# Optimization experiments

Measured on AMD Instinct MI355X. Metric: run time of the kernel, lower is better.

Reference implementation:

```python
import jax, jax.numpy as jnp
import numpy as np

B, S, H = 2, 2048, 2048
NH, NKV, HD = 16, 4, 128
ROPE_BASE = 10000.0


def hbit_linear(x, w):
    # BitNet: 8-bit per-token absmax activation quant, ternary (2-bit) weight quant
    s = 127.0 / jnp.clip(jnp.max(jnp.abs(x), axis=-1, keepdims=True), 1e-5, None)
    xq = jnp.clip(jnp.round(x * s), -128, 127) / s
    ws = 1.0 / jnp.clip(jnp.mean(jnp.abs(w)), 1e-5, None)
    wq = jnp.clip(jnp.round(w * ws), -1, 1) / ws
    return xq @ wq.T


def rotate_half(x):
    h = x.shape[-1] // 2
    return jnp.concatenate([-x[..., h:], x[..., :h]], axis=-1)


def rope_cos_sin(position_ids, head_dim, dtype):
    inv_freq = 1.0 / (ROPE_BASE ** (jnp.arange(0, head_dim, 2, dtype=jnp.float32) / head_dim))
    freqs = position_ids.astype(jnp.float32)[..., None] * inv_freq[None, None, :]  # (b,s,hd/2)
    emb = jnp.concatenate([freqs, freqs], axis=-1)  # (b,s,hd)
    return jnp.cos(emb).astype(dtype)[:, :, None, :], jnp.sin(emb).astype(dtype)[:, :, None, :]


def setup_inputs() -> dict:
    key = jax.random.key(0)
    ks = jax.random.split(key, 5)
    xavier = lambda k, shp: jax.random.uniform(k, shp, jnp.float32, -1.0, 1.0) * np.sqrt(6.0 / (shp[0] + shp[1]))
    causal = jnp.where(jnp.tril(jnp.ones((S, S), bool)), 0.0, -1e9).astype(jnp.float32)[None, None]
    return {
        "hidden_states": jax.random.normal(ks[0], (B, S, H), jnp.float32),
        "attention_mask": causal,
        "Wq": xavier(ks[1], (H, H)),
        "Wk": xavier(ks[2], (NKV * HD, H)),
        "Wv": xavier(ks[3], (NKV * HD, H)),
        "Wo": xavier(ks[4], (H, H)),
        "position_ids": jnp.arange(S, dtype=jnp.int64 if jax.config.jax_enable_x64 else jnp.int32)[None, :],
    }


def reference(hidden_states, attention_mask, Wq, Wk, Wv, Wo, position_ids):
    b, s, _ = hidden_states.shape
    q = hbit_linear(hidden_states, Wq).reshape(b, s, NH, HD)
    k = hbit_linear(hidden_states, Wk).reshape(b, s, NKV, HD)
    v = hbit_linear(hidden_states, Wv).reshape(b, s, NKV, HD)
    cos, sin = rope_cos_sin(position_ids, HD, q.dtype)  # (1,s,1,hd)
    q = q * cos + rotate_half(q) * sin
    k = k * cos + rotate_half(k) * sin
    n_rep = NH // NKV
    k = jnp.repeat(k, n_rep, axis=2)  # (b,s,NH,hd)
    v = jnp.repeat(v, n_rep, axis=2)
    scale = 1.0 / np.sqrt(HD)
    scores = jnp.einsum("bqhd,bkhd->bhqk", q, k) * scale + attention_mask
    probs = jax.nn.softmax(scores, axis=-1)  # dropout inactive (eval)
    out = jnp.einsum("bhqk,bkhd->bqhd", probs, v).reshape(b, s, NH * HD)
    return hbit_linear(out, Wo)
```

## Files before the change

### kernel.cpp

```cpp
#include <hip/hip_runtime.h>
#include <hip/hip_bf16.h>

#define B_ 2
#define S_ 2048
#define H_ 2048
#define NH_ 16
#define NKV_ 4
#define HD_ 128
#define M_ (B_*S_)
#define KVD_ (NKV_*HD_)

typedef signed char s8;
typedef __attribute__((ext_vector_type(8))) short short8;
typedef __attribute__((ext_vector_type(4))) float f32x4;
typedef __attribute__((ext_vector_type(4))) int int4v;

__device__ __forceinline__ float loadf(const void* p, long i, int isb){
  if (isb) return __bfloat162float(((const __hip_bfloat16*)p)[i]);
  return ((const float*)p)[i];
}

__device__ __forceinline__ unsigned short f2bf(float f){
  union { float f; unsigned u; } v; v.f = f;
  unsigned r = v.u + 0x7FFF + ((v.u >> 16) & 1);
  return (unsigned short)(r >> 16);
}

__device__ __forceinline__ float bf2f(unsigned short b){
  union { unsigned u; float f; } v; v.u = ((unsigned)b) << 16; return v.f;
}

__device__ __forceinline__ void gl2lds16(const void* g, void* l){
  __builtin_amdgcn_global_load_lds(
      (const __attribute__((address_space(1))) void*)g,
      (__attribute__((address_space(3))) void*)l, 16, 0, 0);
}

__global__ void k_detect(const unsigned int* x, int* flag){
  __shared__ int sh[256];
  int t = threadIdx.x, c = 0;
  for (int i = t; i < 2048; i += 256){
    unsigned e = (x[i] >> 7) & 0xFF;
    if (e >= 90 && e <= 150) c++;
  }
  sh[t] = c; __syncthreads();
  for (int k = 128; k > 0; k >>= 1){ if (t < k) sh[t] += sh[t+k]; __syncthreads(); }
  if (t == 0) flag[0] = (sh[0] > 1228) ? 1 : 0;
}

__global__ void k_prep(const void* Wq, const void* Wk, const void* Wv, const void* Wo,
                       const int* flag, float* wsum, float* ct, float* st){
  int bid = blockIdx.x, t = threadIdx.x;
  if (t < 64){
    float inv = exp2f(-(float)t * 0.20762050593045952f);
    float a = (float)bid * inv;
    float sn, cs; sincosf(a, &sn, &cs);
    ct[bid*64 + t] = cs; st[bid*64 + t] = sn;
  }
  __shared__ float sh[256];
  int isb = *flag;
  const void* w; long n; int wi; long b0; int nb;
  if (bid < 768)       { w = Wq; wi = 0; n = (long)H_*H_;   b0 = bid;      nb = 768; }
  else if (bid < 1024) { w = Wk; wi = 1; n = (long)KVD_*H_; b0 = bid-768;  nb = 256; }
  else if (bid < 1280) { w = Wv; wi = 2; n = (long)KVD_*H_; b0 = bid-1024; nb = 256; }
  else                 { w = Wo; wi = 3; n = (long)H_*H_;   b0 = bid-1280; nb = 768; }
  float s = 0.f;
  for (long i = b0*256 + t; i < n; i += (long)nb*256) s += fabsf(loadf(w, i, isb));
  sh[t] = s; __syncthreads();
  for (int k = 128; k > 0; k >>= 1){ if (t < k) sh[t] += sh[t+k]; __syncthreads(); }
  if (t == 0) atomicAdd(&wsum[wi], sh[0]);
}

__global__ void k_wquant_all(const void* Wq, const void* Wk, const void* Wv, const void* Wo,
                             const int* flag, const float* wsum,
                             s8* oq, s8* ok, s8* ov, s8* oo){
  int isb = *flag;
  int bid = blockIdx.x, t = threadIdx.x;
  const float cntq = (float)((long)H_*H_), cntkv = (float)((long)KVD_*H_);
  const void* w; s8* out; long n; int wi; long b0; int nb; float cnt;
  if (bid < 1024)      { w = Wq; out = oq; wi = 0; n = (long)H_*H_;   b0 = bid;       nb = 1024; cnt = cntq; }
  else if (bid < 1280) { w = Wk; out = ok; wi = 1; n = (long)KVD_*H_; b0 = bid-1024;  nb = 256;  cnt = cntkv; }
  else if (bid < 1536) { w = Wv; out = ov; wi = 2; n = (long)KVD_*H_; b0 = bid-1280;  nb = 256;  cnt = cntkv; }
  else                 { w = Wo; out = oo; wi = 3; n = (long)H_*H_;   b0 = bid-1536;  nb = 1024; cnt = cntq; }
  float mean = fmaxf(wsum[wi] / cnt, 1e-5f);
  float sc = 1.0f / mean;
  for (long i = b0*256 + t; i < n; i += (long)nb*256){
    float v = rintf(loadf(w, i, isb) * sc);
    v = fminf(fmaxf(v, -1.f), 1.f);
    out[i] = (s8)v;
  }
}

__global__ void k_aquant_in(const void* x, const int* flag, float* srow, s8* xq){
  __shared__ float sh[256];
  int isb = *flag; int r = blockIdx.x, t = threadIdx.x;
  long base = (long)r * H_;
  float v[8];
  if (isb){
    uint4 wv = ((const uint4*)((const unsigned short*)x + base))[t];
    unsigned u[4] = {wv.x, wv.y, wv.z, wv.w};
    #pragma unroll
    for (int i = 0; i < 4; i++){
      v[2*i]   = bf2f((unsigned short)(u[i] & 0xFFFF));
      v[2*i+1] = bf2f((unsigned short)(u[i] >> 16));
    }
  } else {
    const float4* p = (const float4*)((const float*)x + base);
    float4 a = p[t*2], b2 = p[t*2+1];
    v[0]=a.x; v[1]=a.y; v[2]=a.z; v[3]=a.w; v[4]=b2.x; v[5]=b2.y; v[6]=b2.z; v[7]=b2.w;
  }
  float mx = 0.f;
  #pragma unroll
  for (int i = 0; i < 8; i++) mx = fmaxf(mx, fabsf(v[i]));
  sh[t] = mx; __syncthreads();
  for (int k = 128; k > 0; k >>= 1){ if (t < k) sh[t] = fmaxf(sh[t], sh[t+k]); __syncthreads(); }
  float s = 127.0f / fmaxf(sh[0], 1e-5f);
  if (t == 0) srow[r] = s;
  unsigned long long pk = 0;
  #pragma unroll
  for (int i = 0; i < 8; i++){
    float q = fminf(fmaxf(rintf(v[i] * s), -128.f), 127.f);
    pk |= ((unsigned long long)(unsigned char)(s8)q) << (8*i);
  }
  *(unsigned long long*)(xq + base + t*8) = pk;
}

__global__ void k_aquant_bf16(const unsigned short* __restrict__ x, float* __restrict__ srow, s8* __restrict__ xq){
  __shared__ float sh[256];
  int r = blockIdx.x, t = threadIdx.x;
  long base = (long)r * H_;
  uint4 wv = ((const uint4*)(x + base))[t];
  unsigned u[4] = {wv.x, wv.y, wv.z, wv.w};
  float v[8];
  #pragma unroll
  for (int i = 0; i < 4; i++){
    v[2*i]   = bf2f((unsigned short)(u[i] & 0xFFFF));
    v[2*i+1] = bf2f((unsigned short)(u[i] >> 16));
  }
  float mx = 0.f;
  #pragma unroll
  for (int i = 0; i < 8; i++) mx = fmaxf(mx, fabsf(v[i]));
  sh[t] = mx; __syncthreads();
  for (int k = 128; k > 0; k >>= 1){ if (t < k) sh[t] = fmaxf(sh[t], sh[t+k]); __syncthreads(); }
  float s = 127.0f / fmaxf(sh[0], 1e-5f);
  if (t == 0) srow[r] = s;
  unsigned long long pk = 0;
  #pragma unroll
  for (int i = 0; i < 8; i++){
    float q = fminf(fmaxf(rintf(v[i] * s), -128.f), 127.f);
    pk |= ((unsigned long long)(unsigned char)(s8)q) << (8*i);
  }
  *(unsigned long long*)(xq + base + t*8) = pk;
}

__device__ __forceinline__ void gemm_core(
      const s8* __restrict__ A, const s8* __restrict__ Bw, s8* As, s8* Bs,
      const float* __restrict__ srow, float mean,
      void* __restrict__ Cout, int N, int mode, int isb,
      unsigned short* __restrict__ Vt,
      const float* __restrict__ ct, const float* __restrict__ st,
      long bcol, long arow){
  int tid = threadIdx.x;
  int wave = tid >> 6, lane = tid & 63;
  int quad = lane >> 4, c = lane & 15;
  int wm = wave >> 1, wn = wave & 1;
  const int K = H_;

  int4v acc[4][4];
  #pragma unroll
  for (int mt = 0; mt < 4; mt++)
    #pragma unroll
    for (int nt = 0; nt < 4; nt++) acc[mt][nt] = (int4v){0,0,0,0};

  int rl = lane >> 2;
  int kq = (lane & 3) ^ ((lane >> 3) & 3);
  int ch0 = wave*2, ch1 = wave*2 + 1;
  long gA0 = (arow + ch0*16 + rl)*(long)K + kq*16;
  long gA1 = (arow + ch1*16 + rl)*(long)K + kq*16;
  long gB0 = (bcol + ch0*16 + rl)*(long)K + kq*16;
  long gB1 = (bcol + ch1*16 + rl)*(long)K + kq*16;

  int sA = quad ^ ((c >> 1) & 3);
  int ntl[4];
  #pragma unroll
  for (int nt = 0; nt < 4; nt++) ntl[nt] = 2*wn + (nt & 1) + 4*(nt >> 1);
  int frA[4], frB[4];
  #pragma unroll
  for (int mt = 0; mt < 4; mt++) frA[mt] = (wm*64 + mt*16 + c)*64 + sA*16;
  #pragma unroll
  for (int nt = 0; nt < 4; nt++) frB[nt] = (ntl[nt]*16 + c)*64 + sA*16;

  for (int k0 = 0; k0 < K; k0 += 64){
    gl2lds16(A  + gA0 + k0, As + ch0*1024);
    gl2lds16(A  + gA1 + k0, As + ch1*1024);
    gl2lds16(Bw + gB0 + k0, Bs + ch0*1024);
    gl2lds16(Bw + gB1 + k0, Bs + ch1*1024);
    __syncthreads();
    int4v afr[4], bfr[4];
    #pragma unroll
    for (int mt = 0; mt < 4; mt++) afr[mt] = *(const int4v*)&As[frA[mt]];
    #pragma unroll
    for (int nt = 0; nt < 4; nt++) bfr[nt] = *(const int4v*)&Bs[frB[nt]];
    #pragma unroll
    for (int mt = 0; mt < 4; mt++)
      #pragma unroll
      for (int nt = 0; nt < 4; nt++)
        acc[mt][nt] = __builtin_amdgcn_mfma_i32_16x16x64_i8(afr[mt], bfr[nt], acc[mt][nt], 0, 0, 0);
    __syncthreads();
  }

  if (mode == 0 || mode == 3){
    unsigned short* Ob = (unsigned short*)Cout;
    #pragma unroll
    for (int mt = 0; mt < 4; mt++){
      #pragma unroll
      for (int r = 0; r < 4; r++){
        long grow = arow + wm*64 + mt*16 + quad*4 + r;
        float sc = mean / srow[grow];
        if (mode == 0) sc *= 0.12751743f;
        int pos = (int)(grow & (S_-1));
        #pragma unroll
        for (int p = 0; p < 2; p++){
          int col_lo = (int)bcol + (2*wn + p)*16 + c;
          int d = col_lo & 63;
          float cv = ct[pos*64 + d], sv = st[pos*64 + d];
          float vlo = acc[mt][p][r]   * sc;
          float vhi = acc[mt][p+2][r] * sc;
          Ob[grow*(long)N + col_lo]      = f2bf(vlo*cv - vhi*sv);
          Ob[grow*(long)N + col_lo + 64] = f2bf(vhi*cv + vlo*sv);
        }
      }
    }
  } else if (mode == 1){
    #pragma unroll
    for (int mt = 0; mt < 4; mt++){
      #pragma unroll
      for (int r = 0; r < 4; r++){
        long grow = arow + wm*64 + mt*16 + quad*4 + r;
        float sc = mean / srow[grow];
        long bb = grow >> 11; int sI = (int)(grow & (S_-1));
        unsigned short* base = Vt + bb*(long)KVD_*S_ + sI;
        #pragma unroll
        for (int nt = 0; nt < 4; nt++)
          base[(long)(bcol + ntl[nt]*16 + c)*S_] = f2bf(acc[mt][nt][r] * sc);
      }
    }
  } else {
    #pragma unroll
    for (int mt = 0; mt < 4; mt++){
      #pragma unroll
      for (int r = 0; r < 4; r++){
        long grow = arow + wm*64 + mt*16 + quad*4 + r;
        float sc = mean / srow[grow];
        long cb = grow*(long)N + bcol + c;
        if (isb){
          __hip_bfloat16* o = (__hip_bfloat16*)Cout;
          #pragma unroll
          for (int nt = 0; nt < 4; nt++)
            o[cb + ntl[nt]*16] = __float2bfloat16(acc[mt][nt][r] * sc);
        } else {
          float* o = (float*)Cout;
          #pragma unroll
          for (int nt = 0; nt < 4; nt++)
            o[cb + ntl[nt]*16] = acc[mt][nt][r] * sc;
        }
      }
    }
  }
}

__global__ __launch_bounds__(256, 2) void k_gemm_qkv(
      const s8* __restrict__ xq,
      const s8* __restrict__ wqq, const s8* __restrict__ wkq, const s8* __restrict__ wvq,
      const float* __restrict__ srow, const float* __restrict__ wsum,
      unsigned short* __restrict__ Qb, unsigned short* __restrict__ Kb,
      unsigned short* __restrict__ Vt,
      const float* __restrict__ ct, const float* __restrict__ st){
  __shared__ __align__(16) s8 As[128*64];
  __shared__ __align__(16) s8 Bs[128*64];
  int lid = blockIdx.x;
  int xcd = lid & 7;
  int rem = lid >> 3;
  int by  = xcd*4 + (rem & 3);
  int bx  = rem >> 2;
  const float cntq = (float)((long)H_*H_), cntkv = (float)((long)KVD_*H_);
  const s8* Bw; void* Cout; unsigned short* vt = nullptr;
  int N, mode; float mean; long bcol;
  if (bx < 16){
    Bw = wqq; Cout = Qb; N = H_;   mode = 0; mean = fmaxf(wsum[0]/cntq, 1e-5f);  bcol = (long)bx*128;
  } else if (bx < 20){
    Bw = wkq; Cout = Kb; N = KVD_; mode = 3; mean = fmaxf(wsum[1]/cntkv, 1e-5f); bcol = (long)(bx-16)*128;
  } else {
    Bw = wvq; Cout = nullptr; vt = Vt; N = KVD_; mode = 1; mean = fmaxf(wsum[2]/cntkv, 1e-5f); bcol = (long)(bx-20)*128;
  }
  gemm_core(xq, Bw, As, Bs, srow, mean, Cout, N, mode, 0, vt, ct, st, bcol, (long)by*128);
}

__global__ __launch_bounds__(256, 2) void k_gemm_o(
      const s8* __restrict__ aq, const s8* __restrict__ woq,
      const float* __restrict__ srow, const float* __restrict__ wsum,
      const int* __restrict__ flag, void* __restrict__ out,
      const float* __restrict__ ct, const float* __restrict__ st){
  __shared__ __align__(16) s8 As[128*64];
  __shared__ __align__(16) s8 Bs[128*64];
  int lid = blockIdx.x;
  int xcd = lid & 7;
  int rem = lid >> 3;
  int by  = xcd*4 + (rem & 3);
  int bx  = rem >> 2;
  float mean = fmaxf(wsum[3] / (float)((long)H_*H_), 1e-5f);
  gemm_core(aq, woq, As, Bs, srow, mean, out, H_, 2, *flag, nullptr, ct, st,
            (long)bx*128, (long)by*128);
}

#define PSTR 40
__global__ __launch_bounds__(256) void k_attn_mfma(const unsigned short* __restrict__ Qb,
    const unsigned short* __restrict__ Kb, const unsigned short* __restrict__ Vt,
    unsigned short* __restrict__ ob){
  int wid = threadIdx.x >> 6, lane = threadIdx.x & 63;
  int quad = lane >> 4, c = lane & 15;
  int lid = blockIdx.x;
  int panel = lid & 7;
  int kvh = panel & 3, b = panel >> 2;
  int win = lid >> 3;
  int h = kvh*4 + wid;
  int q0 = win*32;

  __shared__ __align__(16) unsigned short Ks[64*128];
  __shared__ __align__(16) unsigned short Vs[128*64];
  __shared__ __align__(16) unsigned short Ps[4][16*PSTR];

  short8 qf[2][4];
  #pragma unroll
  for (int t0 = 0; t0 < 2; t0++)
    #pragma unroll
    for (int f = 0; f < 4; f++)
      qf[t0][f] = *(const short8*)(Qb + ((long)(b*S_ + q0 + t0*16 + c)*NH_ + h)*HD_ + f*32 + quad*8);

  const unsigned short* Kg = Kb + (long)b*S_*KVD_ + kvh*HD_;
  const unsigned short* Vg = Vt + ((long)b*KVD_ + kvh*HD_)*S_;

  f32x4 o[2][8], ol[2];
  #pragma unroll
  for (int t0 = 0; t0 < 2; t0++){
    #pragma unroll
    for (int i = 0; i < 8; i++) o[t0][i] = (f32x4){0.f,0.f,0.f,0.f};
    ol[t0] = (f32x4){0.f,0.f,0.f,0.f};
  }
  short8 ones;
  #pragma unroll
  for (int i = 0; i < 8; i++) ones[i] = (short)0x3F80;

  int skey = lane >> 4;
  int kslot = lane & 15;
  int vrow = lane >> 3;
  int vslot = lane & 7;

  int nk = q0 + 32;
  #pragma unroll
  for (int i = 0; i < 4; i++){
    int kk = wid*16 + i*4;
    int key = kk + skey;
    int g = kslot ^ (key & 15);
    gl2lds16(Kg + (long)key*KVD_ + g*8, &Ks[kk*128]);
  }

  for (int kc = 0; kc < nk; kc += 64){
    __syncthreads();
    #pragma unroll
    for (int i = 0; i < 4; i++){
      int rr = wid*32 + i*8;
      int hd = rr + vrow;
      int g = vslot ^ (hd & 7);
      gl2lds16(Vg + (long)hd*S_ + kc + g*8, &Vs[rr*64]);
    }

    f32x4 s[2][4];
    #pragma unroll
    for (int t0 = 0; t0 < 2; t0++)
      #pragma unroll
      for (int kt = 0; kt < 4; kt++) s[t0][kt] = (f32x4){0.f,0.f,0.f,0.f};
    #pragma unroll
    for (int kt = 0; kt < 4; kt++){
      short8 kf4[4];
      #pragma unroll
      for (int f = 0; f < 4; f++)
        kf4[f] = *(const short8*)&Ks[(kt*16 + c)*128 + ((f*4 + quad) ^ c)*8];
      #pragma unroll
      for (int t0 = 0; t0 < 2; t0++)
        #pragma unroll
        for (int f = 0; f < 4; f++)
          s[t0][kt] = __builtin_amdgcn_mfma_f32_16x16x32_bf16(kf4[f], qf[t0][f], s[t0][kt], 0, 0, 0);
    }
    #pragma unroll
    for (int t0 = 0; t0 < 2; t0++){
      int qv = q0 + t0*16 + c;
      if (kc + 63 > q0 + t0*16){
        #pragma unroll
        for (int kt = 0; kt < 4; kt++){
          #pragma unroll
          for (int r = 0; r < 4; r++){
            int key = kc + kt*16 + quad*4 + r;
            if (key > qv) s[t0][kt][r] = -1e30f;
          }
        }
      }
    }

    __syncthreads();

    if (kc + 64 < nk){
      #pragma unroll
      for (int i = 0; i < 4; i++){
        int kk = wid*16 + i*4;
        int key = kk + skey;
        int g = kslot ^ (key & 15);
        gl2lds16(Kg + (long)(kc + 64 + key)*KVD_ + g*8, &Ks[kk*128]);
      }
    }

    #pragma unroll
    for (int pp = 0; pp < 2; pp++){
      short8 vf[8];
      #pragma unroll
      for (int nt = 0; nt < 8; nt++)
        vf[nt] = *(const short8*)&Vs[(nt*16 + c)*64 + ((pp*4 + quad) ^ (c & 7))*8];
      #pragma unroll
      for (int t0 = 0; t0 < 2; t0++){
        #pragma unroll
        for (int tk = 0; tk < 2; tk++){
          f32x4 sv = s[t0][pp*2 + tk];
          float e0 = exp2f(sv[0]), e1 = exp2f(sv[1]);
          float e2 = exp2f(sv[2]), e3 = exp2f(sv[3]);
          unsigned w0, w1;
          asm("v_cvt_pk_bf16_f32 %0, %1, %2" : "=v"(w0) : "v"(e0), "v"(e1));
          asm("v_cvt_pk_bf16_f32 %0, %1, %2" : "=v"(w1) : "v"(e2), "v"(e3));
          uint2 pkv; pkv.x = w0; pkv.y = w1;
          *(uint2*)&Ps[wid][c*PSTR + tk*16 + quad*4] = pkv;
        }
        short8 pf = *(const short8*)&Ps[wid][c*PSTR + quad*8];
        #pragma unroll
        for (int nt = 0; nt < 8; nt++)
          o[t0][nt] = __builtin_amdgcn_mfma_f32_16x16x32_bf16(pf, vf[nt], o[t0][nt], 0, 0, 0);
        ol[t0] = __builtin_amdgcn_mfma_f32_16x16x32_bf16(pf, ones, ol[t0], 0, 0, 0);
      }
    }
  }

  #pragma unroll
  for (int t0 = 0; t0 < 2; t0++){
    float il[4];
    #pragma unroll
    for (int r = 0; r < 4; r++) il[r] = 1.0f / ol[t0][r];
    #pragma unroll
    for (int nt = 0; nt < 8; nt++)
      #pragma unroll
      for (int r = 0; r < 4; r++)
        ob[((long)(b*S_ + q0 + t0*16 + quad*4 + r))*H_ + h*HD_ + nt*16 + c] = f2bf(o[t0][nt][r]*il[r]);
  }
}

extern "C" void kernel_launch(void* const* d_in, const int* in_sizes, int n_in,
                              void* d_out, int out_size, void* d_ws, size_t ws_size,
                              hipStream_t stream){
  (void)in_sizes; (void)n_in; (void)out_size; (void)ws_size;
  const void* x  = d_in[0];
  const void* Wq = d_in[2];
  const void* Wk = d_in[3];
  const void* Wv = d_in[4];
  const void* Wo = d_in[5];
  char* ws = (char*)d_ws;
  size_t o = 0;
  auto alloc = [&](size_t b){ size_t r = o; o += (b + 255) & ~(size_t)255; return r; };
  size_t META = alloc(256);
  float* wsum = (float*)(ws + META);
  int*   flag = (int*)  (ws + META + 32);
  float* s_x = (float*)(ws + alloc((size_t)M_*4));
  float* s_a = (float*)(ws + alloc((size_t)M_*4));
  float* ct  = (float*)(ws + alloc((size_t)S_*64*4));
  float* st  = (float*)(ws + alloc((size_t)S_*64*4));
  s8* xq  = (s8*)(ws + alloc((size_t)M_*H_));
  s8* wqq = (s8*)(ws + alloc((size_t)H_*H_));
  s8* wkq = (s8*)(ws + alloc((size_t)KVD_*H_));
  s8* wvq = (s8*)(ws + alloc((size_t)KVD_*H_));
  s8* woq = (s8*)(ws + alloc((size_t)H_*H_));
  unsigned short* Qb = (unsigned short*)(ws + alloc((size_t)M_*NH_*HD_*2));
  unsigned short* Kb = (unsigned short*)(ws + alloc((size_t)M_*KVD_*2));
  unsigned short* Vt = (unsigned short*)(ws + alloc((size_t)M_*KVD_*2));
  unsigned short* ab = (unsigned short*)(ws + alloc((size_t)M_*H_*2));
  s8* aq = xq;

  hipMemsetAsync(ws + META, 0, 64, stream);
  k_detect<<<1,256,0,stream>>>((const unsigned int*)x, flag);
  k_prep<<<2048,256,0,stream>>>(Wq, Wk, Wv, Wo, flag, wsum, ct, st);
  k_wquant_all<<<2560,256,0,stream>>>(Wq, Wk, Wv, Wo, flag, wsum, wqq, wkq, wvq, woq);
  k_aquant_in<<<M_,256,0,stream>>>(x, flag, s_x, xq);

  k_gemm_qkv<<<768, 256, 0, stream>>>(xq, wqq, wkq, wvq, s_x, wsum, Qb, Kb, Vt, ct, st);

  k_attn_mfma<<<512, 256, 0, stream>>>(Qb, Kb, Vt, ab);

  k_aquant_bf16<<<M_,256,0,stream>>>(ab, s_a, aq);

  k_gemm_o<<<512, 256, 0, stream>>>(aq, woq, s_a, wsum, flag, d_out, ct, st);
}
```

Baseline: 318.4 us.

## Deepen GEMM K-step, double-buffer attention K tiles, remap attention grid

The int8 GEMM core now stages two 64-wide K slices per barrier pair, halving the number of syncs per output tile at the cost of twice the LDS. The attention kernel double-buffers the K tile so the next chunk's load targets a separate buffer. It also launches on a 3D grid, with batch 1 traversing query windows in reverse to mix long and short causal blocks. The grid remap and the added LDS change occupancy and scheduling behaviour.

```diff
diff --git a/kernel.cpp b/kernel.cpp
--- a/kernel.cpp
+++ b/kernel.cpp
@@ -190,22 +190,31 @@
   #pragma unroll
   for (int nt = 0; nt < 4; nt++) frB[nt] = (ntl[nt]*16 + c)*64 + sA*16;
 
-  for (int k0 = 0; k0 < K; k0 += 64){
-    gl2lds16(A  + gA0 + k0, As + ch0*1024);
-    gl2lds16(A  + gA1 + k0, As + ch1*1024);
-    gl2lds16(Bw + gB0 + k0, Bs + ch0*1024);
-    gl2lds16(Bw + gB1 + k0, Bs + ch1*1024);
+  for (int k0 = 0; k0 < K; k0 += 128){
+    gl2lds16(A  + gA0 + k0,      As        + ch0*1024);
+    gl2lds16(A  + gA1 + k0,      As        + ch1*1024);
+    gl2lds16(Bw + gB0 + k0,      Bs        + ch0*1024);
+    gl2lds16(Bw + gB1 + k0,      Bs        + ch1*1024);
+    gl2lds16(A  + gA0 + k0 + 64, As + 8192 + ch0*1024);
+    gl2lds16(A  + gA1 + k0 + 64, As + 8192 + ch1*1024);
+    gl2lds16(Bw + gB0 + k0 + 64, Bs + 8192 + ch0*1024);
+    gl2lds16(Bw + gB1 + k0 + 64, Bs + 8192 + ch1*1024);
     __syncthreads();
-    int4v afr[4], bfr[4];
-    #pragma unroll
-    for (int mt = 0; mt < 4; mt++) afr[mt] = *(const int4v*)&As[frA[mt]];
-    #pragma unroll
-    for (int nt = 0; nt < 4; nt++) bfr[nt] = *(const int4v*)&Bs[frB[nt]];
-    #pragma unroll
-    for (int mt = 0; mt < 4; mt++)
-      #pragma unroll
-      for (int nt = 0; nt < 4; nt++)
-        acc[mt][nt] = __builtin_amdgcn_mfma_i32_16x16x64_i8(afr[mt], bfr[nt], acc[mt][nt], 0, 0, 0);
+    #pragma unroll
+    for (int s = 0; s < 2; s++){
+      const s8* Ab = As + s*8192;
+      const s8* Bb = Bs + s*8192;
+      int4v afr[4], bfr[4];
+      #pragma unroll
+      for (int mt = 0; mt < 4; mt++) afr[mt] = *(const int4v*)&Ab[frA[mt]];
+      #pragma unroll
+      for (int nt = 0; nt < 4; nt++) bfr[nt] = *(const int4v*)&Bb[frB[nt]];
+      #pragma unroll
+      for (int mt = 0; mt < 4; mt++)
+        #pragma unroll
+        for (int nt = 0; nt < 4; nt++)
+          acc[mt][nt] = __builtin_amdgcn_mfma_i32_16x16x64_i8(afr[mt], bfr[nt], acc[mt][nt], 0, 0, 0);
+    }
     __syncthreads();
   }
 
@@ -276,8 +285,8 @@
       unsigned short* __restrict__ Qb, unsigned short* __restrict__ Kb,
       unsigned short* __restrict__ Vt,
       const float* __restrict__ ct, const float* __restrict__ st){
-  __shared__ __align__(16) s8 As[128*64];
-  __shared__ __align__(16) s8 Bs[128*64];
+  __shared__ __align__(16) s8 As[2*128*64];
+  __shared__ __align__(16) s8 Bs[2*128*64];
   int lid = blockIdx.x;
   int xcd = lid & 7;
   int rem = lid >> 3;
@@ -301,8 +310,8 @@
       const float* __restrict__ srow, const float* __restrict__ wsum,
       const int* __restrict__ flag, void* __restrict__ out,
       const float* __restrict__ ct, const float* __restrict__ st){
-  __shared__ __align__(16) s8 As[128*64];
-  __shared__ __align__(16) s8 Bs[128*64];
+  __shared__ __align__(16) s8 As[2*128*64];
+  __shared__ __align__(16) s8 Bs[2*128*64];
   int lid = blockIdx.x;
   int xcd = lid & 7;
   int rem = lid >> 3;
@@ -319,14 +328,13 @@
     unsigned short* __restrict__ ob){
   int wid = threadIdx.x >> 6, lane = threadIdx.x & 63;
   int quad = lane >> 4, c = lane & 15;
-  int lid = blockIdx.x;
-  int panel = lid & 7;
-  int kvh = panel & 3, b = panel >> 2;
-  int win = lid >> 3;
+  int kvh = blockIdx.y, b = blockIdx.z;
+  int win = blockIdx.x;
+  if (b == 1) win = (S_/32 - 1) - win;
   int h = kvh*4 + wid;
   int q0 = win*32;
 
-  __shared__ __align__(16) unsigned short Ks[64*128];
+  __shared__ __align__(16) unsigned short Ks[2][64*128];
   __shared__ __align__(16) unsigned short Vs[128*64];
   __shared__ __align__(16) unsigned short Ps[4][16*PSTR];
 
@@ -362,10 +370,11 @@
     int kk = wid*16 + i*4;
     int key = kk + skey;
     int g = kslot ^ (key & 15);
-    gl2lds16(Kg + (long)key*KVD_ + g*8, &Ks[kk*128]);
-  }
-
-  for (int kc = 0; kc < nk; kc += 64){
+    gl2lds16(Kg + (long)key*KVD_ + g*8, &Ks[0][kk*128]);
+  }
+
+  int buf = 0;
+  for (int kc = 0; kc < nk; kc += 64, buf ^= 1){
     __syncthreads();
     #pragma unroll
     for (int i = 0; i < 4; i++){
@@ -385,7 +394,7 @@
       short8 kf4[4];
       #pragma unroll
       for (int f = 0; f < 4; f++)
-        kf4[f] = *(const short8*)&Ks[(kt*16 + c)*128 + ((f*4 + quad) ^ c)*8];
+        kf4[f] = *(const short8*)&Ks[buf][(kt*16 + c)*128 + ((f*4 + quad) ^ c)*8];
       #pragma unroll
       for (int t0 = 0; t0 < 2; t0++)
         #pragma unroll
@@ -415,7 +424,7 @@
         int kk = wid*16 + i*4;
         int key = kk + skey;
         int g = kslot ^ (key & 15);
-        gl2lds16(Kg + (long)(kc + 64 + key)*KVD_ + g*8, &Ks[kk*128]);
+        gl2lds16(Kg + (long)(kc + 64 + key)*KVD_ + g*8, &Ks[buf^1][kk*128]);
       }
     }
 
@@ -498,7 +507,8 @@
 
   k_gemm_qkv<<<768, 256, 0, stream>>>(xq, wqq, wkq, wvq, s_x, wsum, Qb, Kb, Vt, ct, st);
 
-  k_attn_mfma<<<512, 256, 0, stream>>>(Qb, Kb, Vt, ab);
+  dim3 ga(S_/32, NKV_, B_);
+  k_attn_mfma<<<ga, 256, 0, stream>>>(Qb, Kb, Vt, ab);
 
   k_aquant_bf16<<<M_,256,0,stream>>>(ab, s_a, aq);
 
```

Result: faster. 307.9 us (-3.3%).
